# Optimization experiments

Hardware: AMD Instinct MI355X
Metric: run time of the kernel (lower is better)

## Reference

```python
import jax, jax.numpy as jnp
import numpy as np

THETA0 = 3.0
THETA = 5.0


def _edt(bg):
    """Exact Euclidean distance transform.
    bg: [B,H,W] bool, True where distance is 0 (the 'background'/feature set).
    Returns [B,H,W] float32 distance of every pixel to the nearest True pixel.
    Separable two-pass algorithm: 1D pass along H via scan, then exact
    min over column offsets along W (Meijster lower-envelope done densely).
    """
    B, H, W = bg.shape
    big = jnp.float32(H + W)
    f = bg.astype(jnp.float32)
    xs = jnp.moveaxis(f, 1, 0)  # [H,B,W] scan over rows

    def step(carry, row):
        d = jnp.where(row > 0, 0.0, carry + 1.0)
        return d, d

    init = jnp.full((B, W), big, jnp.float32)
    _, gf = jax.lax.scan(step, init, xs)                  # top-down
    _, gb = jax.lax.scan(step, init, xs, reverse=True)    # bottom-up
    g = jnp.minimum(gf, gb)            # [H,B,W] 1D vertical distance
    g = jnp.moveaxis(g, 0, 1)          # [B,H,W]
    g2 = jnp.minimum(g, big) ** 2
    col = jnp.arange(W, dtype=jnp.float32)
    off2 = (col[:, None] - col[None, :]) ** 2             # [j,k]
    # d2[b,i,j] = min_k g2[b,i,k] + (j-k)^2   -> [B,H,W,W] intermediate
    d2 = jnp.min(g2[:, :, None, :] + off2[None, None, :, :], axis=-1)
    return jnp.sqrt(d2)


def reference(predictions, targets):
    # predictions: [B,1,H,W] logits; targets: [B,1,H,W] binary masks
    t = targets[:, 0]                                   # [B,H,W]
    fg = t > 0.5
    dist_pos = _edt(~fg)   # distance_transform_edt(target): dist to nearest 0
    dist_neg = _edt(fg)    # distance_transform_edt(1-target): dist to nearest 1
    dist_map = jnp.where(fg, dist_pos, -dist_neg)
    # weight = 1 / (1 + exp((|d| - theta0)/theta)) == sigmoid(-(|d|-theta0)/theta)
    weight = jax.nn.sigmoid(-(jnp.abs(dist_map) - THETA0) / THETA)[:, None]  # [B,1,H,W]
    # numerically stable BCE-with-logits == BCE(sigmoid(x), t)
    x = predictions
    bce = jnp.maximum(x, 0.0) - x * targets + jnp.log1p(jnp.exp(-jnp.abs(x)))
    return jnp.mean(bce * weight)


def setup_inputs() -> dict:
    key = jax.random.key(0)
    k1, k2 = jax.random.split(key)
    B, C, H, W = 8, 1, 256, 256
    predictions = jax.random.normal(k1, (B, C, H, W), dtype=jnp.float32)
    targets = jax.random.randint(k2, (B, C, H, W), 0, 2).astype(jnp.float32)
    return {"predictions": predictions, "targets": targets}
```

## Files before the change

kernel.cpp:

```cpp
#include <hip/hip_runtime.h>
#include <math.h>

#define BB 8
#define HH 256
#define WW 256
#define NPIX (BB*HH*WW)
#define BIGI 512
#define BIGBIG (1<<20)

#define P_OFF   (2 * NPIX)
#define P_STRIDE 32
#define C_OFF   (P_OFF + 16 * P_STRIDE)

__global__ __launch_bounds__(256) void pack_masks(
    const float* __restrict__ tgt,
    float* __restrict__ ws) {
  if (blockIdx.x == 0) {
    if (threadIdx.x < 16) ws[P_OFF + threadIdx.x * P_STRIDE] = 0.0f;
    if (threadIdx.x == 16) ((int*)ws)[C_OFF] = 0;
  }

  unsigned int* maskws = (unsigned int*)ws;
  int j = threadIdx.x >> 5;
  int c = threadIdx.x & 31;
  int im = blockIdx.x >> 3;
  int w = ((blockIdx.x & 7) << 5) + c;
  size_t ibase = (size_t)im * (HH * WW) + w;

  unsigned int m = 0;
#pragma unroll
  for (int i = 0; i < 32; ++i) {
    float t = tgt[ibase + (size_t)(32 * j + i) * WW];
    m |= (t > 0.5f ? 1u : 0u) << i;
  }
  maskws[im * 2048 + j * 256 + w] = m;
}

#define ENV_GROUP(kk) { float4 v = s4[kk];                        \
    float D0 = fw - (float)(4 * (kk));                            \
    d2 = fminf(d2, fmaf(D0, D0, v.x));                            \
    float D1 = D0 - 1.0f; d2 = fminf(d2, fmaf(D1, D1, v.y));      \
    float D2 = D0 - 2.0f; d2 = fminf(d2, fmaf(D2, D2, v.z));      \
    float D3 = D0 - 3.0f; d2 = fminf(d2, fmaf(D3, D3, v.w)); }

__global__ __launch_bounds__(1024) void edt_row_loss4(
    const float* __restrict__ pred,
    float* __restrict__ ws,
    float* __restrict__ out) {
  __shared__ __align__(16) float lA[4][WW];
  __shared__ __align__(16) float lB[4][WW];
  __shared__ float wsum[16];
  __shared__ int lastFlag;

  const unsigned int* maskws = (const unsigned int*)ws;
  float* partials = ws + P_OFF;
  int* counter = ((int*)ws) + C_OFF;

  int tid = threadIdx.x;
  int im = blockIdx.x >> 6;
  int rg = blockIdx.x & 63;
  int r = tid >> 8;
  int w = tid & 255;
  int R = 4 * rg + r;
  int k = R >> 5;
  int rr = R & 31;

  unsigned int M[8];
#pragma unroll
  for (int j = 0; j < 8; ++j) M[j] = maskws[im * 2048 + j * 256 + w];

  float x = pred[(size_t)blockIdx.x * (4 * WW) + tid];

  int fcA = BIGBIG, fcB = BIGBIG, bcA = BIGBIG, bcB = BIGBIG;
  {
    int cA = BIGBIG, cB = BIGBIG;
#pragma unroll
    for (int j = 0; j < 8; ++j) {
      if (j == k) { fcA = cA; fcB = cB; }
      unsigned int a = ~M[j], bm = M[j];
      cA = a  ? (int)__builtin_clz(a)  : cA + 32;
      cB = bm ? (int)__builtin_clz(bm) : cB + 32;
    }
  }
  {
    int cA = BIGBIG, cB = BIGBIG;
#pragma unroll
    for (int j = 7; j >= 0; --j) {
      if (j == k) { bcA = cA; bcB = cB; }
      unsigned int a = ~M[j], bm = M[j];
      cA = a  ? (int)__builtin_ctz(a)  : cA + 32;
      cB = bm ? (int)__builtin_ctz(bm) : cB + 32;
    }
  }

  unsigned int mk = M[k];
  bool fg = (mk >> rr) & 1u;
  float t = fg ? 1.0f : 0.0f;

  {
    unsigned int mA = ~mk;
    unsigned int xx = mA << (31 - rr);
    unsigned int yy = mA >> rr;
    int df = xx ? (int)__builtin_clz(xx) : (rr + 1 + fcA);
    int db = yy ? (int)__builtin_ctz(yy) : (32 - rr + bcA);
    int d = min(min(df, db), BIGI);
    lA[r][w] = (float)(d * d);
  }
  {
    unsigned int mB = mk;
    unsigned int xx = mB << (31 - rr);
    unsigned int yy = mB >> rr;
    int df = xx ? (int)__builtin_clz(xx) : (rr + 1 + fcB);
    int db = yy ? (int)__builtin_ctz(yy) : (32 - rr + bcB);
    int d = min(min(df, db), BIGI);
    lB[r][w] = (float)(d * d);
  }
  __syncthreads();

  const float4* s4 = (const float4*)(fg ? lA[r] : lB[r]);

  int w0 = w & ~63;
  int kc0 = w0 >> 2;
  float fw = (float)w;
  float d2 = 1e30f;

#pragma unroll 4
  for (int kk = kc0; kk < kc0 + 16; ++kk) ENV_GROUP(kk);

  int kL = kc0 - 1;
  int kR = kc0 + 16;
  for (int iter = 0; iter < 16; ++iter) {
    int bL = (kL >= 0) ? (w0 - 4 * kL - 3) : 100000;
    int bR = (kR <= 63) ? (4 * kR - w0 - 63) : 100000;
    int bb = min(bL, bR);
    float bb2 = (float)bb * (float)bb;
    if (__all(d2 <= bb2)) break;
    if (kL >= 0) { ENV_GROUP(kL); kL--; }
    if (kR <= 63) { ENV_GROUP(kR); kR++; }
  }

  float dd = sqrtf(d2);
  float weight = 1.0f / (1.0f + __expf((dd - 3.0f) * 0.2f));
  float bce = fmaxf(x, 0.0f) - x * t + log1pf(__expf(-fabsf(x)));
  float c = bce * weight * (1.0f / (float)NPIX);

#pragma unroll
  for (int off = 32; off > 0; off >>= 1) c += __shfl_down(c, off, 64);
  if ((tid & 63) == 0) wsum[tid >> 6] = c;
  __syncthreads();

  if (tid < 64) {
    float v = (tid < 16) ? wsum[tid] : 0.0f;
#pragma unroll
    for (int off = 8; off > 0; off >>= 1) v += __shfl_down(v, off, 64);
    if (tid == 0) {
      atomicAdd(&partials[(blockIdx.x & 15) * P_STRIDE], v);
      __threadfence();
      int done = atomicAdd(counter, 1);
      lastFlag = (done == (int)gridDim.x - 1) ? 1 : 0;
    }
  }
  __syncthreads();

  if (lastFlag && tid < 64) {
    float v = (tid < 16) ? atomicAdd(&partials[tid * P_STRIDE], 0.0f) : 0.0f;
#pragma unroll
    for (int off = 8; off > 0; off >>= 1) v += __shfl_down(v, off, 64);
    if (tid == 0) out[0] = v;
  }
}

extern "C" void kernel_launch(void* const* d_in, const int* in_sizes, int n_in,
                              void* d_out, int out_size, void* d_ws, size_t ws_size,
                              hipStream_t stream) {
  const float* pred = (const float*)d_in[0];
  const float* tgt  = (const float*)d_in[1];
  float* out = (float*)d_out;
  float* ws  = (float*)d_ws;

  pack_masks<<<dim3(64), dim3(256), 0, stream>>>(tgt, ws);
  edt_row_loss4<<<dim3(512), dim3(1024), 0, stream>>>(pred, ws, out);
}
```

Baseline: 71.08 us.

## Transpose packed mask layout, split pack rows across threads, per-thread envelope search

The pack kernel now runs 512 threads, with each thread packing 16 rows instead of 32. The two halves are merged through shared memory and stored in a column-major layout of 8 words per column. The EDT kernel can then load each column's 8 mask words with two uint4 loads instead of 8 strided loads. The row envelope search now starts at each thread's own 4-wide group and grows outward with a per-thread bound. Before, it scanned a fixed 16-group window per 64-column block. This cuts the usual min-scan work for random masks, but may add divergence in the early-exit loop.

```diff
diff --git a/kernel.cpp b/kernel.cpp
--- a/kernel.cpp
+++ b/kernel.cpp
@@ -12,38 +12,47 @@
 #define P_STRIDE 32
 #define C_OFF   (P_OFF + 16 * P_STRIDE)
 
-__global__ __launch_bounds__(256) void pack_masks(
+__global__ __launch_bounds__(512) void pack_masks_t(
     const float* __restrict__ tgt,
     float* __restrict__ ws) {
+  __shared__ unsigned int halfw[2][8][32];
+
   if (blockIdx.x == 0) {
     if (threadIdx.x < 16) ws[P_OFF + threadIdx.x * P_STRIDE] = 0.0f;
     if (threadIdx.x == 16) ((int*)ws)[C_OFF] = 0;
   }
 
-  unsigned int* maskws = (unsigned int*)ws;
-  int j = threadIdx.x >> 5;
-  int c = threadIdx.x & 31;
+  int tid = threadIdx.x;
+  int h = tid >> 8;
+  int j = (tid >> 5) & 7;
+  int c = tid & 31;
   int im = blockIdx.x >> 3;
   int w = ((blockIdx.x & 7) << 5) + c;
-  size_t ibase = (size_t)im * (HH * WW) + w;
+  size_t ib = (size_t)im * (HH * WW) + (size_t)(32 * j + 16 * h) * WW + w;
 
   unsigned int m = 0;
 #pragma unroll
-  for (int i = 0; i < 32; ++i) {
-    float t = tgt[ibase + (size_t)(32 * j + i) * WW];
+  for (int i = 0; i < 16; ++i) {
+    float t = tgt[ib + (size_t)i * WW];
     m |= (t > 0.5f ? 1u : 0u) << i;
   }
-  maskws[im * 2048 + j * 256 + w] = m;
+  halfw[h][j][c] = m;
+  __syncthreads();
+
+  if (h == 0) {
+    unsigned int full = halfw[0][j][c] | (halfw[1][j][c] << 16);
+    ((unsigned int*)ws)[im * 2048 + w * 8 + j] = full;
+  }
 }
 
-#define ENV_GROUP(kk) { float4 v = s4[kk];                        \
-    float D0 = fw - (float)(4 * (kk));                            \
+#define ENV_G(gg) { float4 v = s4[gg];                            \
+    float D0 = fw - (float)((gg) << 2);                           \
     d2 = fminf(d2, fmaf(D0, D0, v.x));                            \
     float D1 = D0 - 1.0f; d2 = fminf(d2, fmaf(D1, D1, v.y));      \
     float D2 = D0 - 2.0f; d2 = fminf(d2, fmaf(D2, D2, v.z));      \
     float D3 = D0 - 3.0f; d2 = fminf(d2, fmaf(D3, D3, v.w)); }
 
-__global__ __launch_bounds__(1024) void edt_row_loss4(
+__global__ __launch_bounds__(1024) void edt_row_loss5(
     const float* __restrict__ pred,
     float* __restrict__ ws,
     float* __restrict__ out) {
@@ -65,9 +74,9 @@
   int k = R >> 5;
   int rr = R & 31;
 
-  unsigned int M[8];
-#pragma unroll
-  for (int j = 0; j < 8; ++j) M[j] = maskws[im * 2048 + j * 256 + w];
+  const uint4* mp = (const uint4*)(maskws + im * 2048 + w * 8);
+  uint4 mlo = mp[0], mhi = mp[1];
+  unsigned int M[8] = {mlo.x, mlo.y, mlo.z, mlo.w, mhi.x, mhi.y, mhi.z, mhi.w};
 
   float x = pred[(size_t)blockIdx.x * (4 * WW) + tid];
 
@@ -107,9 +116,8 @@
     lA[r][w] = (float)(d * d);
   }
   {
-    unsigned int mB = mk;
-    unsigned int xx = mB << (31 - rr);
-    unsigned int yy = mB >> rr;
+    unsigned int xx = mk << (31 - rr);
+    unsigned int yy = mk >> rr;
     int df = xx ? (int)__builtin_clz(xx) : (rr + 1 + fcB);
     int db = yy ? (int)__builtin_ctz(yy) : (32 - rr + bcB);
     int d = min(min(df, db), BIGI);
@@ -118,25 +126,20 @@
   __syncthreads();
 
   const float4* s4 = (const float4*)(fg ? lA[r] : lB[r]);
-
-  int w0 = w & ~63;
-  int kc0 = w0 >> 2;
+  int gc = w >> 2;
   float fw = (float)w;
   float d2 = 1e30f;
 
-#pragma unroll 4
-  for (int kk = kc0; kk < kc0 + 16; ++kk) ENV_GROUP(kk);
-
-  int kL = kc0 - 1;
-  int kR = kc0 + 16;
-  for (int iter = 0; iter < 16; ++iter) {
-    int bL = (kL >= 0) ? (w0 - 4 * kL - 3) : 100000;
-    int bR = (kR <= 63) ? (4 * kR - w0 - 63) : 100000;
-    int bb = min(bL, bR);
+  ENV_G(gc);
+  for (int dlt = 1; dlt <= 16; ++dlt) {
+    int gl = gc - dlt, gr = gc + dlt;
+    int bl = (gl >= 0) ? (w - 4 * gl - 3) : 100000;
+    int br = (gr <= 63) ? (4 * gr - w) : 100000;
+    int bb = min(bl, br);
     float bb2 = (float)bb * (float)bb;
     if (__all(d2 <= bb2)) break;
-    if (kL >= 0) { ENV_GROUP(kL); kL--; }
-    if (kR <= 63) { ENV_GROUP(kR); kR++; }
+    if (gl >= 0) ENV_G(gl);
+    if (gr <= 63) ENV_G(gr);
   }
 
   float dd = sqrtf(d2);
@@ -178,6 +181,6 @@
   float* out = (float*)d_out;
   float* ws  = (float*)d_ws;
 
-  pack_masks<<<dim3(64), dim3(256), 0, stream>>>(tgt, ws);
-  edt_row_loss4<<<dim3(512), dim3(1024), 0, stream>>>(pred, ws, out);
+  pack_masks_t<<<dim3(64), dim3(512), 0, stream>>>(tgt, ws);
+  edt_row_loss5<<<dim3(512), dim3(1024), 0, stream>>>(pred, ws, out);
 }
```

After: 69.90 us. About the same (-1.7%).
